# Optimization experiments

Measured on AMD Instinct MI355X. Metric: run time of the kernel, lower is better.

Reference implementation:

```python
import jax, jax.numpy as jnp
import numpy as np

N_NODES = 4096
N_EDGES = 131072
D_EDGE = 128
N_HEADS = 8


def setup_inputs() -> dict:
    key = jax.random.key(0)
    k1, k2, k3, k4 = jax.random.split(key, 4)
    edge_index = jax.random.randint(k1, (2, N_EDGES), 0, N_NODES, dtype=jnp.int32)
    edge_attr = jax.random.normal(k2, (N_EDGES, D_EDGE), dtype=jnp.float32)
    W = jax.random.normal(k3, (D_EDGE, N_HEADS), dtype=jnp.float32) * (1.0 / np.sqrt(D_EDGE))
    b = jax.random.normal(k4, (N_HEADS,), dtype=jnp.float32) * 0.01
    return {"edge_index": edge_index, "edge_attr": edge_attr, "W": W, "b": b,
            "num_nodes": N_NODES}


def reference(edge_index, edge_attr, W, b, num_nodes):
    # Linear edge projection: [E, D_edge] @ [D_edge, H] + [H] -> [E, H]
    scores = edge_attr @ W + b
    u = edge_index[0]
    v = edge_index[1]
    H = W.shape[1]
    # Dense bias [H, N, N]; non-edge positions stay 0.
    bias = jnp.zeros((H, num_nodes, num_nodes), dtype=scores.dtype)
    bias = bias.at[:, u, v].set(scores.T)
    return bias
```

## Files before the change

### kernel.cpp

```cpp
#include <hip/hip_runtime.h>

#define N_NODES 4096
#define N_EDGES 131072
#define D_EDGE  128
#define N_HEADS 8

#define WS_SCORES_OFF  0
#define WS_WINNER_OFF  ((size_t)N_EDGES * N_HEADS * sizeof(float))

__global__ void edgebias_scores_winner(const int* __restrict__ edge_index,
                                       const float* __restrict__ edge_attr,
                                       const float* __restrict__ W,
                                       const float* __restrict__ b,
                                       float* __restrict__ scores,
                                       int* __restrict__ winner) {
    __shared__ float Ws[D_EDGE * N_HEADS];
    __shared__ float bs[N_HEADS];
    for (int i = threadIdx.x; i < D_EDGE * N_HEADS; i += blockDim.x)
        Ws[i] = W[i];
    if (threadIdx.x < N_HEADS) bs[threadIdx.x] = b[threadIdx.x];
    __syncthreads();

    int e = blockIdx.x * blockDim.x + threadIdx.x;
    if (e >= N_EDGES) return;

    float acc[N_HEADS];
    #pragma unroll
    for (int h = 0; h < N_HEADS; ++h) acc[h] = bs[h];

    const float4* row = (const float4*)(edge_attr + (size_t)e * D_EDGE);
    #pragma unroll 8
    for (int j = 0; j < D_EDGE / 4; ++j) {
        float4 a = row[j];
        int d = j * 4;
        #pragma unroll
        for (int h = 0; h < N_HEADS; ++h) {
            acc[h] += a.x * Ws[(d + 0) * N_HEADS + h]
                    + a.y * Ws[(d + 1) * N_HEADS + h]
                    + a.z * Ws[(d + 2) * N_HEADS + h]
                    + a.w * Ws[(d + 3) * N_HEADS + h];
        }
    }

    float4 s0 = make_float4(acc[0], acc[1], acc[2], acc[3]);
    float4 s1 = make_float4(acc[4], acc[5], acc[6], acc[7]);
    ((float4*)scores)[(size_t)e * 2 + 0] = s0;
    ((float4*)scores)[(size_t)e * 2 + 1] = s1;

    int u = edge_index[e];
    int v = edge_index[N_EDGES + e];
    atomicMax(&winner[u * N_NODES + v], e + 1);
}

__global__ void edgebias_scatter(const int* __restrict__ edge_index,
                                 const float* __restrict__ scores,
                                 const int* __restrict__ winner,
                                 float* __restrict__ out) {
    int t = blockIdx.x * blockDim.x + threadIdx.x;
    int e = t >> 3;
    int h = t & 7;
    int u = edge_index[e];
    int v = edge_index[N_EDGES + e];
    size_t cell = (size_t)u * N_NODES + v;
    if (winner[cell] == e + 1)
        out[(size_t)h * N_NODES * N_NODES + cell] = scores[t];
}

extern "C" void kernel_launch(void* const* d_in, const int* in_sizes, int n_in,
                              void* d_out, int out_size, void* d_ws, size_t ws_size,
                              hipStream_t stream) {
    const int*   edge_index = (const int*)  d_in[0];
    const float* edge_attr  = (const float*)d_in[1];
    const float* W          = (const float*)d_in[2];
    const float* b          = (const float*)d_in[3];
    float* out = (float*)d_out;

    float* scores = (float*)((char*)d_ws + WS_SCORES_OFF);
    int*   winner = (int*)  ((char*)d_ws + WS_WINNER_OFF);

    hipMemsetAsync(d_out, 0, (size_t)N_HEADS * N_NODES * N_NODES * sizeof(float), stream);
    hipMemsetAsync(winner, 0, (size_t)N_NODES * N_NODES * sizeof(int), stream);

    edgebias_scores_winner<<<dim3((N_EDGES + 255) / 256), dim3(256), 0, stream>>>(
        edge_index, edge_attr, W, b, scores, winner);

    edgebias_scatter<<<dim3((N_EDGES * N_HEADS) / 256), dim3(256), 0, stream>>>(
        edge_index, scores, winner, out);
}
```

Baseline: 653.7 us.

## Replace zero-fill plus scatter with dense paint kernel driven by winner map

Removes the full memset of the output and the sparse per-edge scatter, replacing them with a kernel that walks every cell of the winner map and writes all heads (zero or score) in one dense pass. This avoids writing the large output twice and drops the random scattered stores. In exchange it reads the entire winner array and gathers scores for occupied cells.

```diff
diff --git a/kernel.cpp b/kernel.cpp
--- a/kernel.cpp
+++ b/kernel.cpp
@@ -4,6 +4,7 @@
 #define N_EDGES 131072
 #define D_EDGE  128
 #define N_HEADS 8
+#define N_CELLS ((size_t)N_NODES * N_NODES)
 
 #define WS_SCORES_OFF  0
 #define WS_WINNER_OFF  ((size_t)N_EDGES * N_HEADS * sizeof(float))
@@ -42,28 +43,45 @@
         }
     }
 
-    float4 s0 = make_float4(acc[0], acc[1], acc[2], acc[3]);
-    float4 s1 = make_float4(acc[4], acc[5], acc[6], acc[7]);
-    ((float4*)scores)[(size_t)e * 2 + 0] = s0;
-    ((float4*)scores)[(size_t)e * 2 + 1] = s1;
+    ((float4*)scores)[(size_t)e * 2 + 0] = make_float4(acc[0], acc[1], acc[2], acc[3]);
+    ((float4*)scores)[(size_t)e * 2 + 1] = make_float4(acc[4], acc[5], acc[6], acc[7]);
 
     int u = edge_index[e];
     int v = edge_index[N_EDGES + e];
     atomicMax(&winner[u * N_NODES + v], e + 1);
 }
 
-__global__ void edgebias_scatter(const int* __restrict__ edge_index,
-                                 const float* __restrict__ scores,
-                                 const int* __restrict__ winner,
-                                 float* __restrict__ out) {
-    int t = blockIdx.x * blockDim.x + threadIdx.x;
-    int e = t >> 3;
-    int h = t & 7;
-    int u = edge_index[e];
-    int v = edge_index[N_EDGES + e];
-    size_t cell = (size_t)u * N_NODES + v;
-    if (winner[cell] == e + 1)
-        out[(size_t)h * N_NODES * N_NODES + cell] = scores[t];
+__global__ void edgebias_paint(const float* __restrict__ scores,
+                               const int* __restrict__ winner,
+                               float* __restrict__ out) {
+    size_t t = (size_t)blockIdx.x * blockDim.x + threadIdx.x;
+    int4 w = ((const int4*)winner)[t];
+
+    float sc[4][N_HEADS];
+    #pragma unroll
+    for (int c = 0; c < 4; ++c)
+        #pragma unroll
+        for (int h = 0; h < N_HEADS; ++h)
+            sc[c][h] = 0.0f;
+
+    int we[4] = {w.x, w.y, w.z, w.w};
+    #pragma unroll
+    for (int c = 0; c < 4; ++c) {
+        if (we[c] != 0) {
+            const float4* sp = (const float4*)scores + (size_t)(we[c] - 1) * 2;
+            float4 lo = sp[0];
+            float4 hi = sp[1];
+            sc[c][0] = lo.x; sc[c][1] = lo.y; sc[c][2] = lo.z; sc[c][3] = lo.w;
+            sc[c][4] = hi.x; sc[c][5] = hi.y; sc[c][6] = hi.z; sc[c][7] = hi.w;
+        }
+    }
+
+    float4* out4 = (float4*)out;
+    #pragma unroll
+    for (int h = 0; h < N_HEADS; ++h) {
+        out4[(size_t)h * (N_CELLS / 4) + t] =
+            make_float4(sc[0][h], sc[1][h], sc[2][h], sc[3][h]);
+    }
 }
 
 extern "C" void kernel_launch(void* const* d_in, const int* in_sizes, int n_in,
@@ -78,12 +96,11 @@
     float* scores = (float*)((char*)d_ws + WS_SCORES_OFF);
     int*   winner = (int*)  ((char*)d_ws + WS_WINNER_OFF);
 
-    hipMemsetAsync(d_out, 0, (size_t)N_HEADS * N_NODES * N_NODES * sizeof(float), stream);
-    hipMemsetAsync(winner, 0, (size_t)N_NODES * N_NODES * sizeof(int), stream);
+    hipMemsetAsync(winner, 0, N_CELLS * sizeof(int), stream);
 
     edgebias_scores_winner<<<dim3((N_EDGES + 255) / 256), dim3(256), 0, stream>>>(
         edge_index, edge_attr, W, b, scores, winner);
 
-    edgebias_scatter<<<dim3((N_EDGES * N_HEADS) / 256), dim3(256), 0, stream>>>(
-        edge_index, scores, winner, out);
+    edgebias_paint<<<dim3((unsigned)(N_CELLS / 4 / 256)), dim3(256), 0, stream>>>(
+        scores, winner, out);
 }
```

Measured after the change: 622.9 us. 4.7% less time.
